# Performance work log

Measured on AMD Instinct MI355X. Metric: run time of the kernel, lower is better.

## Reference

```python
import jax, jax.numpy as jnp
import numpy as np

N_NODES = 50000
N_EDGES = 800000
DIM = 64
BN_EPS = 1e-5
L2_EPS = 1e-12


def setup_inputs() -> dict:
    key = jax.random.key(0)
    k1, k2, k3, k4 = jax.random.split(key, 4)
    x = jax.random.normal(k1, (N_NODES, DIM), dtype=jnp.float32)
    edge_index = jax.random.randint(k2, (2, N_EDGES), 0, N_NODES, dtype=jnp.int64)
    W = jax.random.normal(k3, (DIM, DIM), dtype=jnp.float32) * (1.0 / np.sqrt(DIM))
    b = jax.random.normal(k4, (DIM,), dtype=jnp.float32) * 0.02
    gamma = jnp.ones((DIM,), dtype=jnp.float32)
    beta = jnp.zeros((DIM,), dtype=jnp.float32)
    return {"x": x, "edge_index": edge_index, "W": W, "b": b, "gamma": gamma, "beta": beta}


def reference(x, edge_index, W, b, gamma, beta):
    # GCNConv: x' = D^{-1/2} (A + I) D^{-1/2} X W + b  (self-loops added, edge weight 1)
    N = x.shape[0]
    src, dst = edge_index[0], edge_index[1]
    h = x @ W  # [N, dim_out]
    # degree including self-loop
    deg = jnp.ones((N,), x.dtype).at[dst].add(1.0)
    dinv = jax.lax.rsqrt(deg)
    # self-loop contribution: norm_ii = dinv[i]^2
    out = h * (dinv * dinv)[:, None]
    # edge contributions: norm_ij = dinv[src] * dinv[dst], scatter-add to dst
    norm = dinv[src] * dinv[dst]  # [E]
    out = out.at[dst].add(norm[:, None] * h[src])
    out = out + b
    # BatchNorm1d (training mode: biased batch stats)
    mean = out.mean(axis=0)
    var = ((out - mean) ** 2).mean(axis=0)
    out = (out - mean) * jax.lax.rsqrt(var + BN_EPS) * gamma + beta
    # ReLU
    out = jax.nn.relu(out)
    # F.normalize(p=2, dim=1)
    nrm = jnp.sqrt(jnp.sum(out * out, axis=1, keepdims=True))
    out = out / jnp.maximum(nrm, L2_EPS)
    return out
```

## Files before the change

kernel.cpp:

```cpp
#include <hip/hip_runtime.h>

#define DIM 64
#define BN_EPS 1e-5f
#define L2_EPS 1e-12f
#define CAP 64

__global__ __launch_bounds__(256) void k_gemm(const float* __restrict__ x,
                                              const float* __restrict__ W,
                                              float* __restrict__ h, int N) {
    __shared__ float Ws[DIM][DIM];
    __shared__ float xs[16][DIM];
    int tid = threadIdx.x;
    for (int i = tid; i < DIM * DIM; i += 256) Ws[i >> 6][i & 63] = W[i];
    int tx = tid & 63, ty = tid >> 6;
    const float4* __restrict__ x4 = (const float4*)x;
    for (int r0 = blockIdx.x * 16; r0 < N; r0 += gridDim.x * 16) {
        __syncthreads();
        ((float4*)xs)[tid] = x4[r0 * 16 + tid];
        __syncthreads();
        float a0 = 0.f, a1 = 0.f, a2 = 0.f, a3 = 0.f;
#pragma unroll
        for (int k = 0; k < DIM; ++k) {
            float wv = Ws[k][tx];
            a0 = fmaf(xs[ty][k],      wv, a0);
            a1 = fmaf(xs[ty + 4][k],  wv, a1);
            a2 = fmaf(xs[ty + 8][k],  wv, a2);
            a3 = fmaf(xs[ty + 12][k], wv, a3);
        }
        h[(r0 + ty) * DIM + tx]      = a0;
        h[(r0 + ty + 4) * DIM + tx]  = a1;
        h[(r0 + ty + 8) * DIM + tx]  = a2;
        h[(r0 + ty + 12) * DIM + tx] = a3;
    }
}

__global__ __launch_bounds__(256) void k_reorder(const int* __restrict__ ei,
                                                 int* __restrict__ cur,
                                                 unsigned short* __restrict__ es, int E) {
    int e = blockIdx.x * blockDim.x + threadIdx.x;
    if (e < E) {
        int s = ei[e];
        int d = ei[E + e];
        int p = atomicAdd(&cur[d], 1);
        if (p < CAP) es[(size_t)d * CAP + p] = (unsigned short)s;
    }
}

__global__ __launch_bounds__(256) void k_dinv(const int* __restrict__ cur,
                                              float* __restrict__ dinv, int N) {
    int i = blockIdx.x * blockDim.x + threadIdx.x;
    if (i < N) dinv[i] = rsqrtf((float)(cur[i] + 1));
}

__global__ __launch_bounds__(256) void k_gather(const int* __restrict__ cnt,
                                                const unsigned short* __restrict__ es,
                                                const float* __restrict__ dinv,
                                                const float* __restrict__ h,
                                                const float* __restrict__ b,
                                                float* __restrict__ out, int N) {
    int w = threadIdx.x >> 6;
    int d = blockIdx.x * 4 + w;
    if (d >= N) return;
    int l = threadIdx.x & 63;
    int sub = l >> 4;
    int c = l & 15;
    int deg = min(cnt[d], CAP);
    const float4* __restrict__ h4 = (const float4*)h;
    const unsigned short* __restrict__ row = es + (size_t)d * CAP;
    float4 acc = make_float4(0.f, 0.f, 0.f, 0.f);
    for (int base = 0; base < deg; base += 16) {
#pragma unroll
        for (int u = 0; u < 4; ++u) {
            int k = base + sub + u * 4;
            bool valid = k < deg;
            int s = row[valid ? k : 0];
            float wgt = valid ? dinv[s] : 0.f;
            float4 hv = h4[(size_t)s * 16 + c];
            acc.x = fmaf(wgt, hv.x, acc.x);
            acc.y = fmaf(wgt, hv.y, acc.y);
            acc.z = fmaf(wgt, hv.z, acc.z);
            acc.w = fmaf(wgt, hv.w, acc.w);
        }
    }
    acc.x += __shfl_xor(acc.x, 16, 64); acc.y += __shfl_xor(acc.y, 16, 64);
    acc.z += __shfl_xor(acc.z, 16, 64); acc.w += __shfl_xor(acc.w, 16, 64);
    acc.x += __shfl_xor(acc.x, 32, 64); acc.y += __shfl_xor(acc.y, 32, 64);
    acc.z += __shfl_xor(acc.z, 32, 64); acc.w += __shfl_xor(acc.w, 32, 64);
    if (sub == 0) {
        float dd = dinv[d];
        float4 hd = h4[(size_t)d * 16 + c];
        float4 bv = ((const float4*)b)[c];
        float dd2 = dd * dd;
        float4 o;
        o.x = fmaf(dd2, hd.x, fmaf(dd, acc.x, bv.x));
        o.y = fmaf(dd2, hd.y, fmaf(dd, acc.y, bv.y));
        o.z = fmaf(dd2, hd.z, fmaf(dd, acc.z, bv.z));
        o.w = fmaf(dd2, hd.w, fmaf(dd, acc.w, bv.w));
        ((float4*)out)[(size_t)d * 16 + c] = o;
    }
}

__global__ __launch_bounds__(256) void k_stats(const float* __restrict__ out,
                                               float* __restrict__ stats, int N) {
    int tx = threadIdx.x & 63, ty = threadIdx.x >> 6;
    float s = 0.f, q = 0.f;
    for (int r = blockIdx.x * 4 + ty; r < N; r += gridDim.x * 4) {
        float v = out[r * DIM + tx];
        s += v;
        q = fmaf(v, v, q);
    }
    __shared__ float ls[4][DIM], lq[4][DIM];
    ls[ty][tx] = s;
    lq[ty][tx] = q;
    __syncthreads();
    if (ty == 0) {
        s = ls[0][tx] + ls[1][tx] + ls[2][tx] + ls[3][tx];
        q = lq[0][tx] + lq[1][tx] + lq[2][tx] + lq[3][tx];
        atomicAdd(&stats[tx], s);
        atomicAdd(&stats[DIM + tx], q);
    }
}

__global__ __launch_bounds__(256) void k_final(float* __restrict__ out,
                                               const float* __restrict__ stats,
                                               const float* __restrict__ gamma,
                                               const float* __restrict__ beta,
                                               int N, float invN) {
    int tx = threadIdx.x & 63;
    int r = (blockIdx.x * blockDim.x + threadIdx.x) >> 6;
    if (r >= N) return;
    float mean = stats[tx] * invN;
    float var = fmaf(-mean, mean, stats[DIM + tx] * invN);
    float rstd = rsqrtf(var + BN_EPS);
    float v = out[r * DIM + tx];
    v = (v - mean) * rstd * gamma[tx] + beta[tx];
    v = fmaxf(v, 0.f);
    float q = v * v;
#pragma unroll
    for (int off = 32; off; off >>= 1) q += __shfl_xor(q, off, 64);
    float nrm = sqrtf(q);
    out[r * DIM + tx] = v / fmaxf(nrm, L2_EPS);
}

extern "C" void kernel_launch(void* const* d_in, const int* in_sizes, int n_in,
                              void* d_out, int out_size, void* d_ws, size_t ws_size,
                              hipStream_t stream) {
    const float* x     = (const float*)d_in[0];
    const int*   ei    = (const int*)d_in[1];
    const float* W     = (const float*)d_in[2];
    const float* b     = (const float*)d_in[3];
    const float* gamma = (const float*)d_in[4];
    const float* beta  = (const float*)d_in[5];
    float* out = (float*)d_out;

    const int N = in_sizes[0] / DIM;
    const int E = in_sizes[1] / 2;

    float* wsf = (float*)d_ws;
    const int STATS_OFF = 0;
    const int CUR_OFF   = 256;
    const int DINV_OFF  = CUR_OFF  + ((N + 256) & ~255);
    const int H_OFF     = DINV_OFF + ((N + 256) & ~255);
    const int ES_OFF    = H_OFF + N * DIM;

    float* stats = wsf + STATS_OFF;
    int*   cur   = (int*)(wsf + CUR_OFF);
    float* dinv  = wsf + DINV_OFF;
    float* h     = wsf + H_OFF;
    unsigned short* es = (unsigned short*)(wsf + ES_OFF);

    hipMemsetAsync(wsf, 0, (size_t)(CUR_OFF + N) * sizeof(float), stream);

    k_gemm   <<<1024, 256, 0, stream>>>(x, W, h, N);
    k_reorder<<<(E + 255) / 256, 256, 0, stream>>>(ei, cur, es, E);
    k_dinv   <<<(N + 255) / 256, 256, 0, stream>>>(cur, dinv, N);
    k_gather <<<(N + 3) / 4, 256, 0, stream>>>(cur, es, dinv, h, b, out, N);
    k_stats  <<<512, 256, 0, stream>>>(out, stats, N);
    k_final  <<<(N * 64 + 255) / 256, 256, 0, stream>>>(out, stats, gamma, beta, N, 1.0f / N);
}
```

Measured before the change: 202.6 us.

## Fuse reorder with GEMM, stats into gather, and drop dinv kernel

Merges the edge-bucketing and the x@W GEMM into one launch by giving three quarters of the blocks to edge scatter and one quarter to the GEMM. The separate dinv kernel is removed; degree normalisation is recomputed inline with rsqrt from the counts. BatchNorm statistics are accumulated inside the gather kernel, reduced per block and spread across 32 atomic slots. The final kernel folds mean, rstd, gamma and beta into one scale and shift and uses a grid-stride loop. This cuts three launches and one full pass over the output, at the cost of extra count reads in the gather loop and possible load imbalance between the two roles in the fused kernel.

```diff
diff --git a/kernel.cpp b/kernel.cpp
--- a/kernel.cpp
+++ b/kernel.cpp
@@ -4,19 +4,37 @@
 #define BN_EPS 1e-5f
 #define L2_EPS 1e-12f
 #define CAP 64
+#define SLOTS 32
+#define GBLK 2048
+#define FBLK 2048
 
-__global__ __launch_bounds__(256) void k_gemm(const float* __restrict__ x,
-                                              const float* __restrict__ W,
-                                              float* __restrict__ h, int N) {
+__global__ __launch_bounds__(256) void k_rg(const int* __restrict__ ei,
+                                            int* __restrict__ cur,
+                                            unsigned short* __restrict__ es, int E,
+                                            const float* __restrict__ x,
+                                            const float* __restrict__ W,
+                                            float* __restrict__ h, int N) {
     __shared__ float Ws[DIM][DIM];
     __shared__ float xs[16][DIM];
-    int tid = threadIdx.x;
-    for (int i = tid; i < DIM * DIM; i += 256) Ws[i >> 6][i & 63] = W[i];
-    int tx = tid & 63, ty = tid >> 6;
+    int bid = blockIdx.x;
+    int t = threadIdx.x;
+    if ((bid & 3) != 3) {
+        int rb = (bid >> 2) * 3 + (bid & 3);
+        for (int e = rb * 256 + t; e < E; e += 3072 * 256) {
+            int s = ei[e];
+            int d = ei[E + e];
+            int p = atomicAdd(&cur[d], 1);
+            if (p < CAP) es[(size_t)d * CAP + p] = (unsigned short)s;
+        }
+        return;
+    }
+    int gb = bid >> 2;
+    for (int i = t; i < DIM * DIM; i += 256) Ws[i >> 6][i & 63] = W[i];
+    int tx = t & 63, ty = t >> 6;
     const float4* __restrict__ x4 = (const float4*)x;
-    for (int r0 = blockIdx.x * 16; r0 < N; r0 += gridDim.x * 16) {
+    for (int r0 = gb * 16; r0 < N; r0 += 1024 * 16) {
         __syncthreads();
-        ((float4*)xs)[tid] = x4[r0 * 16 + tid];
+        ((float4*)xs)[t] = x4[r0 * 16 + t];
         __syncthreads();
         float a0 = 0.f, a1 = 0.f, a2 = 0.f, a3 = 0.f;
 #pragma unroll
@@ -34,112 +52,110 @@
     }
 }
 
-__global__ __launch_bounds__(256) void k_reorder(const int* __restrict__ ei,
-                                                 int* __restrict__ cur,
-                                                 unsigned short* __restrict__ es, int E) {
-    int e = blockIdx.x * blockDim.x + threadIdx.x;
-    if (e < E) {
-        int s = ei[e];
-        int d = ei[E + e];
-        int p = atomicAdd(&cur[d], 1);
-        if (p < CAP) es[(size_t)d * CAP + p] = (unsigned short)s;
-    }
-}
-
-__global__ __launch_bounds__(256) void k_dinv(const int* __restrict__ cur,
-                                              float* __restrict__ dinv, int N) {
-    int i = blockIdx.x * blockDim.x + threadIdx.x;
-    if (i < N) dinv[i] = rsqrtf((float)(cur[i] + 1));
-}
-
 __global__ __launch_bounds__(256) void k_gather(const int* __restrict__ cnt,
                                                 const unsigned short* __restrict__ es,
-                                                const float* __restrict__ dinv,
                                                 const float* __restrict__ h,
                                                 const float* __restrict__ b,
-                                                float* __restrict__ out, int N) {
+                                                float* __restrict__ out,
+                                                float* __restrict__ sp, int N) {
     int w = threadIdx.x >> 6;
-    int d = blockIdx.x * 4 + w;
-    if (d >= N) return;
     int l = threadIdx.x & 63;
     int sub = l >> 4;
     int c = l & 15;
-    int deg = min(cnt[d], CAP);
     const float4* __restrict__ h4 = (const float4*)h;
-    const unsigned short* __restrict__ row = es + (size_t)d * CAP;
-    float4 acc = make_float4(0.f, 0.f, 0.f, 0.f);
-    for (int base = 0; base < deg; base += 16) {
+    float4 ss = make_float4(0.f, 0.f, 0.f, 0.f);
+    float4 qq = make_float4(0.f, 0.f, 0.f, 0.f);
+    for (int d0 = blockIdx.x * 4; d0 < N; d0 += GBLK * 4) {
+        int d = d0 + w;
+        if (d < N) {
+            int deg = min(cnt[d], CAP);
+            const unsigned short* __restrict__ row = es + (size_t)d * CAP;
+            float4 acc = make_float4(0.f, 0.f, 0.f, 0.f);
+            for (int base = 0; base < deg; base += 16) {
 #pragma unroll
-        for (int u = 0; u < 4; ++u) {
-            int k = base + sub + u * 4;
-            bool valid = k < deg;
-            int s = row[valid ? k : 0];
-            float wgt = valid ? dinv[s] : 0.f;
-            float4 hv = h4[(size_t)s * 16 + c];
-            acc.x = fmaf(wgt, hv.x, acc.x);
-            acc.y = fmaf(wgt, hv.y, acc.y);
-            acc.z = fmaf(wgt, hv.z, acc.z);
-            acc.w = fmaf(wgt, hv.w, acc.w);
+                for (int u = 0; u < 4; ++u) {
+                    int k = base + sub + u * 4;
+                    bool valid = k < deg;
+                    int s = row[valid ? k : 0];
+                    float wgt = valid ? rsqrtf((float)(cnt[s] + 1)) : 0.f;
+                    float4 hv = h4[(size_t)s * 16 + c];
+                    acc.x = fmaf(wgt, hv.x, acc.x);
+                    acc.y = fmaf(wgt, hv.y, acc.y);
+                    acc.z = fmaf(wgt, hv.z, acc.z);
+                    acc.w = fmaf(wgt, hv.w, acc.w);
+                }
+            }
+            acc.x += __shfl_xor(acc.x, 16, 64); acc.y += __shfl_xor(acc.y, 16, 64);
+            acc.z += __shfl_xor(acc.z, 16, 64); acc.w += __shfl_xor(acc.w, 16, 64);
+            acc.x += __shfl_xor(acc.x, 32, 64); acc.y += __shfl_xor(acc.y, 32, 64);
+            acc.z += __shfl_xor(acc.z, 32, 64); acc.w += __shfl_xor(acc.w, 32, 64);
+            if (sub == 0) {
+                float dd = rsqrtf((float)(cnt[d] + 1));
+                float4 hd = h4[(size_t)d * 16 + c];
+                float4 bv = ((const float4*)b)[c];
+                float dd2 = dd * dd;
+                float4 o;
+                o.x = fmaf(dd2, hd.x, fmaf(dd, acc.x, bv.x));
+                o.y = fmaf(dd2, hd.y, fmaf(dd, acc.y, bv.y));
+                o.z = fmaf(dd2, hd.z, fmaf(dd, acc.z, bv.z));
+                o.w = fmaf(dd2, hd.w, fmaf(dd, acc.w, bv.w));
+                ((float4*)out)[(size_t)d * 16 + c] = o;
+                ss.x += o.x; ss.y += o.y; ss.z += o.z; ss.w += o.w;
+                qq.x = fmaf(o.x, o.x, qq.x); qq.y = fmaf(o.y, o.y, qq.y);
+                qq.z = fmaf(o.z, o.z, qq.z); qq.w = fmaf(o.w, o.w, qq.w);
+            }
         }
     }
-    acc.x += __shfl_xor(acc.x, 16, 64); acc.y += __shfl_xor(acc.y, 16, 64);
-    acc.z += __shfl_xor(acc.z, 16, 64); acc.w += __shfl_xor(acc.w, 16, 64);
-    acc.x += __shfl_xor(acc.x, 32, 64); acc.y += __shfl_xor(acc.y, 32, 64);
-    acc.z += __shfl_xor(acc.z, 32, 64); acc.w += __shfl_xor(acc.w, 32, 64);
+    __shared__ float ls[4][DIM], lq[4][DIM];
     if (sub == 0) {
-        float dd = dinv[d];
-        float4 hd = h4[(size_t)d * 16 + c];
-        float4 bv = ((const float4*)b)[c];
-        float dd2 = dd * dd;
-        float4 o;
-        o.x = fmaf(dd2, hd.x, fmaf(dd, acc.x, bv.x));
-        o.y = fmaf(dd2, hd.y, fmaf(dd, acc.y, bv.y));
-        o.z = fmaf(dd2, hd.z, fmaf(dd, acc.z, bv.z));
-        o.w = fmaf(dd2, hd.w, fmaf(dd, acc.w, bv.w));
-        ((float4*)out)[(size_t)d * 16 + c] = o;
+        ls[w][c * 4 + 0] = ss.x; ls[w][c * 4 + 1] = ss.y;
+        ls[w][c * 4 + 2] = ss.z; ls[w][c * 4 + 3] = ss.w;
+        lq[w][c * 4 + 0] = qq.x; lq[w][c * 4 + 1] = qq.y;
+        lq[w][c * 4 + 2] = qq.z; lq[w][c * 4 + 3] = qq.w;
     }
-}
-
-__global__ __launch_bounds__(256) void k_stats(const float* __restrict__ out,
-                                               float* __restrict__ stats, int N) {
-    int tx = threadIdx.x & 63, ty = threadIdx.x >> 6;
-    float s = 0.f, q = 0.f;
-    for (int r = blockIdx.x * 4 + ty; r < N; r += gridDim.x * 4) {
-        float v = out[r * DIM + tx];
-        s += v;
-        q = fmaf(v, v, q);
-    }
-    __shared__ float ls[4][DIM], lq[4][DIM];
-    ls[ty][tx] = s;
-    lq[ty][tx] = q;
     __syncthreads();
-    if (ty == 0) {
-        s = ls[0][tx] + ls[1][tx] + ls[2][tx] + ls[3][tx];
-        q = lq[0][tx] + lq[1][tx] + lq[2][tx] + lq[3][tx];
-        atomicAdd(&stats[tx], s);
-        atomicAdd(&stats[DIM + tx], q);
+    int t = threadIdx.x;
+    if (t < 128) {
+        int col = t & 63;
+        float v = (t < 64) ? (ls[0][col] + ls[1][col] + ls[2][col] + ls[3][col])
+                           : (lq[0][col] + lq[1][col] + lq[2][col] + lq[3][col]);
+        atomicAdd(&sp[(blockIdx.x & (SLOTS - 1)) * 128 + t], v);
     }
 }
 
 __global__ __launch_bounds__(256) void k_final(float* __restrict__ out,
-                                               const float* __restrict__ stats,
+                                               const float* __restrict__ sp,
                                                const float* __restrict__ gamma,
                                                const float* __restrict__ beta,
                                                int N, float invN) {
-    int tx = threadIdx.x & 63;
-    int r = (blockIdx.x * blockDim.x + threadIdx.x) >> 6;
-    if (r >= N) return;
-    float mean = stats[tx] * invN;
-    float var = fmaf(-mean, mean, stats[DIM + tx] * invN);
-    float rstd = rsqrtf(var + BN_EPS);
-    float v = out[r * DIM + tx];
-    v = (v - mean) * rstd * gamma[tx] + beta[tx];
-    v = fmaxf(v, 0.f);
-    float q = v * v;
+    __shared__ float A[DIM], Bc[DIM];
+    int t = threadIdx.x;
+    if (t < 64) {
+        float s = 0.f, q = 0.f;
+        for (int k = 0; k < SLOTS; ++k) {
+            s += sp[k * 128 + t];
+            q += sp[k * 128 + 64 + t];
+        }
+        float mean = s * invN;
+        float var = fmaf(-mean, mean, q * invN);
+        float rstd = rsqrtf(var + BN_EPS);
+        float a = rstd * gamma[t];
+        A[t] = a;
+        Bc[t] = fmaf(-mean, a, beta[t]);
+    }
+    __syncthreads();
+    int l = t & 63;
+    int w = t >> 6;
+    for (int r = blockIdx.x * 4 + w; r < N; r += FBLK * 4) {
+        float v = out[r * DIM + l];
+        v = fmaf(v, A[l], Bc[l]);
+        v = fmaxf(v, 0.f);
+        float q = v * v;
 #pragma unroll
-    for (int off = 32; off; off >>= 1) q += __shfl_xor(q, off, 64);
-    float nrm = sqrtf(q);
-    out[r * DIM + tx] = v / fmaxf(nrm, L2_EPS);
+        for (int off = 32; off; off >>= 1) q += __shfl_xor(q, off, 64);
+        float nrm = sqrtf(q);
+        out[r * DIM + l] = v / fmaxf(nrm, L2_EPS);
+    }
 }
 
 extern "C" void kernel_launch(void* const* d_in, const int* in_sizes, int n_in,
@@ -157,24 +173,19 @@
     const int E = in_sizes[1] / 2;
 
     float* wsf = (float*)d_ws;
-    const int STATS_OFF = 0;
-    const int CUR_OFF   = 256;
-    const int DINV_OFF  = CUR_OFF  + ((N + 256) & ~255);
-    const int H_OFF     = DINV_OFF + ((N + 256) & ~255);
-    const int ES_OFF    = H_OFF + N * DIM;
+    const int SP_OFF  = 0;
+    const int CUR_OFF = SLOTS * 128;
+    const int H_OFF   = CUR_OFF + ((N + 255) & ~255);
+    const int ES_OFF  = H_OFF + N * DIM;
 
-    float* stats = wsf + STATS_OFF;
-    int*   cur   = (int*)(wsf + CUR_OFF);
-    float* dinv  = wsf + DINV_OFF;
-    float* h     = wsf + H_OFF;
+    float* sp  = wsf + SP_OFF;
+    int*   cur = (int*)(wsf + CUR_OFF);
+    float* h   = wsf + H_OFF;
     unsigned short* es = (unsigned short*)(wsf + ES_OFF);
 
     hipMemsetAsync(wsf, 0, (size_t)(CUR_OFF + N) * sizeof(float), stream);
 
-    k_gemm   <<<1024, 256, 0, stream>>>(x, W, h, N);
-    k_reorder<<<(E + 255) / 256, 256, 0, stream>>>(ei, cur, es, E);
-    k_dinv   <<<(N + 255) / 256, 256, 0, stream>>>(cur, dinv, N);
-    k_gather <<<(N + 3) / 4, 256, 0, stream>>>(cur, es, dinv, h, b, out, N);
-    k_stats  <<<512, 256, 0, stream>>>(out, stats, N);
-    k_final  <<<(N * 64 + 255) / 256, 256, 0, stream>>>(out, stats, gamma, beta, N, 1.0f / N);
+    k_rg    <<<4096, 256, 0, stream>>>(ei, cur, es, E, x, W, h, N);
+    k_gather<<<GBLK, 256, 0, stream>>>(cur, es, h, b, out, sp, N);
+    k_final <<<FBLK, 256, 0, stream>>>(out, sp, gamma, beta, N, 1.0f / N);
 }
```

After: 170.8 us. -15.7%, faster.
